# Kernel optimization log

Hardware: AMD Instinct MI355X
Metric: run time of the kernel (lower is better)

Reference implementation:

```python
import jax, jax.numpy as jnp
import numpy as np

N_NODES = 250_000
N_EDGES = 1_250_000
N_CRY = 50_000
EMB = 200
FEA = 64
HID = 256
N_GRAPH = 3
ELEM_HEADS = 3
CRY_HEADS = 3


def _simple_net(x, w1, b1, w2, b2):
    # SimpleNetwork([d_in, 256, d_out]): Linear -> LeakyReLU -> Linear
    h = jax.nn.leaky_relu(x @ w1 + b1, negative_slope=0.01)
    return h @ w2 + b2


def setup_inputs() -> dict:
    key = jax.random.key(0)
    ks = jax.random.split(key, 32)
    s = 0.05
    inp = {
        # weights strictly positive (fractional stoichiometry weights)
        "elem_weights": jax.random.uniform(ks[0], (N_NODES, 1), jnp.float32) * 0.9 + 0.05,
        "elem_fea": jax.random.normal(ks[1], (N_NODES, EMB), jnp.float32),
        "self_fea_idx": jax.random.randint(ks[2], (N_EDGES,), 0, N_NODES),
        "nbr_fea_idx": jax.random.randint(ks[3], (N_EDGES,), 0, N_NODES),
        "cry_elem_idx": jnp.sort(jax.random.randint(ks[4], (N_NODES,), 0, N_CRY)),
        # embedding: Linear(EMB, FEA-1)
        "emb_w": jax.random.normal(ks[5], (EMB, FEA - 1), jnp.float32) * s,
        "emb_b": jnp.zeros((FEA - 1,), jnp.float32),
        # graph-layer attention heads (n_graph, elem_heads, ...)
        "g_gate_w1": jax.random.normal(ks[6], (N_GRAPH, ELEM_HEADS, 2 * FEA, HID), jnp.float32) * s,
        "g_gate_b1": jnp.zeros((N_GRAPH, ELEM_HEADS, HID), jnp.float32),
        "g_gate_w2": jax.random.normal(ks[7], (N_GRAPH, ELEM_HEADS, HID, 1), jnp.float32) * s,
        "g_gate_b2": jnp.zeros((N_GRAPH, ELEM_HEADS, 1), jnp.float32),
        "g_msg_w1": jax.random.normal(ks[8], (N_GRAPH, ELEM_HEADS, 2 * FEA, HID), jnp.float32) * s,
        "g_msg_b1": jnp.zeros((N_GRAPH, ELEM_HEADS, HID), jnp.float32),
        "g_msg_w2": jax.random.normal(ks[9], (N_GRAPH, ELEM_HEADS, HID, FEA), jnp.float32) * s,
        "g_msg_b2": jnp.zeros((N_GRAPH, ELEM_HEADS, FEA), jnp.float32),
        "g_pow": jax.random.normal(ks[10], (N_GRAPH, ELEM_HEADS), jnp.float32),
        # crystal pooling heads
        "c_gate_w1": jax.random.normal(ks[11], (CRY_HEADS, FEA, HID), jnp.float32) * s,
        "c_gate_b1": jnp.zeros((CRY_HEADS, HID), jnp.float32),
        "c_gate_w2": jax.random.normal(ks[12], (CRY_HEADS, HID, 1), jnp.float32) * s,
        "c_gate_b2": jnp.zeros((CRY_HEADS, 1), jnp.float32),
        "c_msg_w1": jax.random.normal(ks[13], (CRY_HEADS, FEA, HID), jnp.float32) * s,
        "c_msg_b1": jnp.zeros((CRY_HEADS, HID), jnp.float32),
        "c_msg_w2": jax.random.normal(ks[14], (CRY_HEADS, HID, FEA), jnp.float32) * s,
        "c_msg_b2": jnp.zeros((CRY_HEADS, FEA), jnp.float32),
        "c_pow": jax.random.normal(ks[15], (CRY_HEADS,), jnp.float32),
    }
    return inp


def _attn_pool(fea, weights, index, num_segments, gw1, gb1, gw2, gb2, mw1, mb1, mw2, mb2, p):
    # WeightedAttentionPooling: scatter-softmax with (weights ** pow) factor
    gate = _simple_net(fea, gw1, gb1, gw2, gb2)                       # (E, 1)
    gmax = jax.ops.segment_max(gate, index, num_segments=num_segments)
    gate = (weights ** p) * jnp.exp(gate - gmax[index])
    den = jax.ops.segment_sum(gate, index, num_segments=num_segments)
    gate = gate / (den[index] + 1e-10)
    msg = _simple_net(fea, mw1, mb1, mw2, mb2)                        # (E, FEA)
    return jax.ops.segment_sum(gate * msg, index, num_segments=num_segments)


def reference(elem_weights, elem_fea, self_fea_idx, nbr_fea_idx, cry_elem_idx,
              emb_w, emb_b,
              g_gate_w1, g_gate_b1, g_gate_w2, g_gate_b2,
              g_msg_w1, g_msg_b1, g_msg_w2, g_msg_b2, g_pow,
              c_gate_w1, c_gate_b1, c_gate_w2, c_gate_b2,
              c_msg_w1, c_msg_b1, c_msg_w2, c_msg_b2, c_pow):
    n = elem_fea.shape[0]
    x = elem_fea @ emb_w + emb_b                                      # (N, FEA-1)
    x = jnp.concatenate([x, elem_weights], axis=1)                    # (N, FEA)
    w_nbr = elem_weights[nbr_fea_idx]                                 # (M, 1)
    for l in range(g_pow.shape[0]):
        fea = jnp.concatenate([x[self_fea_idx], x[nbr_fea_idx]], axis=1)  # (M, 2*FEA)
        heads = []
        for h in range(g_pow.shape[1]):
            heads.append(_attn_pool(
                fea, w_nbr, self_fea_idx, n,
                g_gate_w1[l, h], g_gate_b1[l, h], g_gate_w2[l, h], g_gate_b2[l, h],
                g_msg_w1[l, h], g_msg_b1[l, h], g_msg_w2[l, h], g_msg_b2[l, h],
                g_pow[l, h]))
        x = jnp.mean(jnp.stack(heads), axis=0) + x                    # residual
    heads = []
    for h in range(c_pow.shape[0]):
        heads.append(_attn_pool(
            x, elem_weights, cry_elem_idx, N_CRY,
            c_gate_w1[h], c_gate_b1[h], c_gate_w2[h], c_gate_b2[h],
            c_msg_w1[h], c_msg_b1[h], c_msg_w2[h], c_msg_b2[h],
            c_pow[h]))
    return jnp.mean(jnp.stack(heads), axis=0)                         # (C, FEA)
```

## Files before the change

### kernel.cpp

```cpp
#include <hip/hip_runtime.h>
#include <math.h>

#define NN 250000
#define NE 1250000
#define NC 50000
#define EMBD 200
#define NCH 245
#define NBLK 22000
#define SSTR ((size_t)NBLK * 64)

typedef unsigned int u32;
typedef unsigned short u16;
typedef short s16x8 __attribute__((ext_vector_type(8)));
typedef float f32x4 __attribute__((ext_vector_type(4)));

__device__ __forceinline__ u16 f2bf(float f) {
    u32 u = __float_as_uint(f);
    return (u16)((u + 0x7FFFu + ((u >> 16) & 1u)) >> 16);
}
__device__ __forceinline__ float bf2f(u16 u) { return __uint_as_float(((u32)u) << 16); }
__device__ __forceinline__ u32 cvtpk(float lo, float hi) {
    u32 r;
    asm("v_cvt_pk_bf16_f32 %0, %1, %2" : "=v"(r) : "v"(lo), "v"(hi));
    return r;
}
__device__ __forceinline__ float lrelu(float v) { return v > 0.f ? v : 0.01f * v; }
__device__ __forceinline__ u32 encf(float f) {
    u32 u = __float_as_uint(f);
    return (u & 0x80000000u) ? ~u : (u | 0x80000000u);
}
__device__ __forceinline__ float decf(u32 k) {
    return __uint_as_float((k & 0x80000000u) ? (k ^ 0x80000000u) : ~k);
}

__global__ void k_pack(const float* __restrict__ src, u16* __restrict__ dst,
                       int K, int N, int nheads)
{
    const int t = blockIdx.x * 256 + threadIdx.x;
    const int F = (K / 32) * (N / 16);
    if (t >= nheads * F * 64) return;
    const int lane = t & 63;
    const int fh = t >> 6;
    const int f = fh % F, head = fh / F;
    const int ng = f % (N / 16), ks = f / (N / 16);
    const int q = lane >> 4, c = lane & 15;
    const float* s = src + (size_t)head * K * N;
    u16 o[8];
    #pragma unroll
    for (int i = 0; i < 8; ++i)
        o[i] = f2bf(s[(size_t)(32 * ks + 8 * q + i) * N + 16 * ng + c]);
    uint4 v;
    v.x = (u32)o[0] | ((u32)o[1] << 16);
    v.y = (u32)o[2] | ((u32)o[3] << 16);
    v.z = (u32)o[4] | ((u32)o[5] << 16);
    v.w = (u32)o[6] | ((u32)o[7] << 16);
    *(uint4*)(dst + (size_t)head * K * N + ((size_t)f * 64 + lane) * 8) = v;
}

__global__ void k_packe(const float* __restrict__ src, u16* __restrict__ dst)
{
    const int t = blockIdx.x * 256 + threadIdx.x;
    if (t >= 28 * 64) return;
    const int lane = t & 63, f = t >> 6;
    const int ng = f & 3, ks = f >> 2;
    const int q = lane >> 4, c = lane & 15;
    u16 o[8];
    #pragma unroll
    for (int i = 0; i < 8; ++i) {
        const int kr = 32 * ks + 8 * q + i;
        const int col = 16 * ng + c;
        o[i] = (kr < EMBD && col < 63) ? f2bf(src[kr * 63 + col]) : (u16)0;
    }
    uint4 v;
    v.x = (u32)o[0] | ((u32)o[1] << 16);
    v.y = (u32)o[2] | ((u32)o[3] << 16);
    v.z = (u32)o[4] | ((u32)o[5] << 16);
    v.w = (u32)o[6] | ((u32)o[7] << 16);
    *(uint4*)(dst + ((size_t)f * 64 + lane) * 8) = v;
}

__global__ void k_pack2(const float* __restrict__ src, u16* __restrict__ dst, int nheads)
{
    const int t = blockIdx.x * 256 + threadIdx.x;
    const int F = 32;
    if (t >= nheads * F * 64) return;
    const int lane = t & 63;
    const int fh = t >> 6;
    const int f = fh % F, head = fh / F;
    const int ks2 = f >> 2, ng = f & 3;
    const int q = lane >> 4, c = lane & 15;
    const int half = ks2 >> 2, k2l = ks2 & 3;
    const float* s = src + (size_t)head * 256 * 64;
    u16 o[8];
    #pragma unroll
    for (int i = 0; i < 8; ++i) {
        const int pl = 32 * k2l + 8 * q + i;
        const int krow = (pl >> 5) * 64 + (2 * half + (pl & 1)) * 16 + ((pl >> 1) & 15);
        o[i] = f2bf(s[(size_t)krow * 64 + 16 * ng + c]);
    }
    uint4 v;
    v.x = (u32)o[0] | ((u32)o[1] << 16);
    v.y = (u32)o[2] | ((u32)o[3] << 16);
    v.z = (u32)o[4] | ((u32)o[5] << 16);
    v.w = (u32)o[6] | ((u32)o[7] << 16);
    *(uint4*)(dst + (size_t)head * 256 * 64 + ((size_t)f * 64 + lane) * 8) = v;
}

__global__ __launch_bounds__(256) void k_embed_mm(
    const float* __restrict__ elem_fea, const float* __restrict__ elem_w,
    const u16* __restrict__ webp, const float* __restrict__ emb_b,
    float* __restrict__ x, u16* __restrict__ xbf)
{
    __shared__ __align__(16) u16 Ahi[64 * 256];
    __shared__ __align__(16) u16 Alo[64 * 256];
    const int tid = threadIdx.x;
    const int n0 = blockIdx.x * 64;

    for (int i = tid; i < 64 * 3; i += 256) {
        const int row = i / 3, j = 25 + i % 3;
        uint4 z; z.x = 0; z.y = 0; z.z = 0; z.w = 0;
        *(uint4*)((char*)Ahi + row * 512 + ((j ^ (row & 7)) * 16)) = z;
        *(uint4*)((char*)Alo + row * 512 + ((j ^ (row & 7)) * 16)) = z;
    }
    for (int i = tid; i < 64 * 50; i += 256) {
        const int row = i / 50, f4 = i % 50;
        const int node = min(n0 + row, NN - 1);
        float4 v = *(const float4*)(elem_fea + (size_t)node * EMBD + f4 * 4);
        const u16 h0 = f2bf(v.x), h1 = f2bf(v.y), h2 = f2bf(v.z), h3 = f2bf(v.w);
        uint2 hi, lo;
        hi.x = (u32)h0 | ((u32)h1 << 16);
        hi.y = (u32)h2 | ((u32)h3 << 16);
        lo.x = (u32)f2bf(v.x - bf2f(h0)) | ((u32)f2bf(v.y - bf2f(h1)) << 16);
        lo.y = (u32)f2bf(v.z - bf2f(h2)) | ((u32)f2bf(v.w - bf2f(h3)) << 16);
        const int off = row * 512 + (((f4 >> 1) ^ (row & 7)) * 16) + (f4 & 1) * 8;
        *(uint2*)((char*)Ahi + off) = hi;
        *(uint2*)((char*)Alo + off) = lo;
    }
    __syncthreads();

    const int w = tid >> 6, lane = tid & 63, q = lane >> 4, c = lane & 15;
    s16x8 B[7];
    #pragma unroll
    for (int ks = 0; ks < 7; ++ks)
        B[ks] = *(const s16x8*)(webp + ((size_t)(ks * 4 + w) * 64 + lane) * 8);
    f32x4 acc[4];
    #pragma unroll
    for (int m = 0; m < 4; ++m) acc[m] = 0.f;
    #pragma unroll
    for (int ks = 0; ks < 7; ++ks) {
        #pragma unroll
        for (int m = 0; m < 4; ++m) {
            const int row = m * 16 + c;
            const int g = (ks * 4 + q) ^ (row & 7);
            s16x8 ah = *(const s16x8*)((const char*)Ahi + row * 512 + g * 16);
            s16x8 al = *(const s16x8*)((const char*)Alo + row * 512 + g * 16);
            acc[m] = __builtin_amdgcn_mfma_f32_16x16x32_bf16(ah, B[ks], acc[m], 0, 0, 0);
            acc[m] = __builtin_amdgcn_mfma_f32_16x16x32_bf16(al, B[ks], acc[m], 0, 0, 0);
        }
    }
    const int col = w * 16 + c;
    const float bv = (col < 63) ? emb_b[col] : 0.f;
    #pragma unroll
    for (int m = 0; m < 4; ++m)
        #pragma unroll
        for (int r = 0; r < 4; ++r) {
            const int node = n0 + m * 16 + q * 4 + r;
            if (node < NN) {
                const float val = (col < 63) ? acc[m][r] + bv : elem_w[node];
                x[(size_t)node * 64 + col] = val;
                xbf[(size_t)node * 64 + col] = f2bf(val);
            }
        }
}

__global__ void k_deg(const int* __restrict__ self_idx, int* __restrict__ deg) {
    int e = blockIdx.x * 256 + threadIdx.x;
    if (e < NE) atomicAdd(&deg[self_idx[e]], 1);
}

__global__ void k_nodepack(const int* __restrict__ deg, int* __restrict__ nstart,
                           int* __restrict__ ctotal)
{
    __shared__ int sdeg[1024];
    __shared__ int sst[1024];
    const int c0 = blockIdx.x << 10;
    const int cnt = min(1024, NN - c0);
    for (int i = threadIdx.x; i < cnt; i += 64) sdeg[i] = deg[c0 + i];
    __syncthreads();
    if (threadIdx.x == 0) {
        int cur = 0;
        for (int i = 0; i < cnt; ++i) {
            int d = sdeg[i];
            if (d > 0 && ((cur & 63) + d > 64)) cur = (cur + 63) & ~63;
            sst[i] = cur;
            cur += d;
        }
        ctotal[blockIdx.x] = (cur + 63) & ~63;
    }
    __syncthreads();
    for (int i = threadIdx.x; i < cnt; i += 64) nstart[c0 + i] = sst[i];
}

__global__ void k_chunkscan(const int* __restrict__ ctotal, int* __restrict__ cbase) {
    __shared__ int s[256];
    int t = threadIdx.x;
    int v = (t < NCH) ? ctotal[t] : 0;
    s[t] = v;
    __syncthreads();
    for (int off = 1; off < 256; off <<= 1) {
        int add = (t >= off) ? s[t - off] : 0;
        __syncthreads();
        s[t] += add;
        __syncthreads();
    }
    if (t < NCH) cbase[t] = s[t] - v;
}

__global__ void k_fill(const int* __restrict__ self_idx, const int* __restrict__ nstart,
                       const int* __restrict__ cbase, int* __restrict__ cursor,
                       int* __restrict__ eslot)
{
    int e = blockIdx.x * 256 + threadIdx.x;
    if (e >= NE) return;
    int n = self_idx[e];
    int r = atomicAdd(&cursor[n], 1);
    eslot[cbase[n >> 10] + nstart[n] + r] = e;
}

__global__ __launch_bounds__(256, 3) void k_lgate(
    const u16* __restrict__ xbf, const int* __restrict__ eslot,
    const int* __restrict__ sidx, const int* __restrict__ nidx,
    const float* __restrict__ elem_w,
    const u16* __restrict__ gw1p, const float* __restrict__ gb1,
    const float* __restrict__ gw2, const float* __restrict__ gpw,
    float* __restrict__ sgf_out)
{
    __shared__ __align__(16) u16 sA[64 * 128];
    __shared__ float sg[4][64];
    __shared__ float gfin[64], tval[64];
    __shared__ float swn[64];
    __shared__ int   snid[64];
    __shared__ short srs[64], sre[64];
    const int tid = threadIdx.x;
    const int base = blockIdx.x * 64;
    if (eslot[base] < 0) return;

    if (tid < 64) {
        int e = eslot[base + tid];
        snid[tid] = (e >= 0) ? sidx[e] : -1;
        swn[tid] = (e >= 0) ? elem_w[nidx[e]] : 1.f;
    }
    for (int i = tid; i < 64 * 16; i += 256) {
        const int row = i >> 4, g = i & 15;
        const int e = eslot[base + row];
        uint4 v; v.x = 0; v.y = 0; v.z = 0; v.w = 0;
        if (e >= 0) {
            const int node = (g < 8) ? sidx[e] : nidx[e];
            v = *(const uint4*)(xbf + (size_t)node * 64 + (g & 7) * 8);
        }
        *(uint4*)((char*)sA + row * 256 + ((g ^ (row & 7)) * 16)) = v;
    }
    __syncthreads();
    if (tid < 64) {
        int n = snid[tid];
        int rs = tid, re = tid + 1;
        if (n >= 0) {
            while (rs > 0 && snid[rs - 1] == n) --rs;
            while (re < 64 && snid[re] == n) ++re;
        }
        srs[tid] = (short)rs; sre[tid] = (short)re;
    }

    const int w = tid >> 6, lane = tid & 63, q = lane >> 4, c = lane & 15;

    #pragma unroll 1
    for (int h = 0; h < 3; ++h) {
        float part[4][4];
        #pragma unroll
        for (int m = 0; m < 4; ++m)
            #pragma unroll
            for (int r = 0; r < 4; ++r) part[m][r] = 0.f;
        const u16* wp = gw1p + (size_t)h * 128 * 256;
        #pragma unroll 1
        for (int half = 0; half < 2; ++half) {
            s16x8 B1[4][2];
            #pragma unroll
            for (int ks = 0; ks < 4; ++ks)
                #pragma unroll
                for (int n2 = 0; n2 < 2; ++n2)
                    B1[ks][n2] = *(const s16x8*)(wp + ((size_t)(ks * 16 + w * 4 + half * 2 + n2) * 64 + lane) * 8);
            f32x4 acc[4][2];
            #pragma unroll
            for (int m = 0; m < 4; ++m) { acc[m][0] = 0.f; acc[m][1] = 0.f; }
            __builtin_amdgcn_s_setprio(1);
            #pragma unroll
            for (int ks = 0; ks < 4; ++ks) {
                s16x8 a[4];
                #pragma unroll
                for (int m = 0; m < 4; ++m) {
                    const int row = m * 16 + c;
                    a[m] = *(const s16x8*)((const char*)sA + row * 256 + (((ks * 4 + q) ^ (row & 7)) * 16));
                }
                #pragma unroll
                for (int n2 = 0; n2 < 2; ++n2)
                    #pragma unroll
                    for (int m = 0; m < 4; ++m)
                        acc[m][n2] = __builtin_amdgcn_mfma_f32_16x16x32_bf16(a[m], B1[ks][n2], acc[m][n2], 0, 0, 0);
            }
            __builtin_amdgcn_s_setprio(0);
            #pragma unroll
            for (int n2 = 0; n2 < 2; ++n2) {
                const int col = w * 64 + (half * 2 + n2) * 16 + c;
                const float b1v = gb1[h * 256 + col];
                const float w2v = gw2[h * 256 + col];
                #pragma unroll
                for (int m = 0; m < 4; ++m)
                    #pragma unroll
                    for (int r = 0; r < 4; ++r)
                        part[m][r] += lrelu(acc[m][n2][r] + b1v) * w2v;
            }
        }
        #pragma unroll
        for (int off = 1; off < 16; off <<= 1)
            #pragma unroll
            for (int m = 0; m < 4; ++m)
                #pragma unroll
                for (int r = 0; r < 4; ++r)
                    part[m][r] += __shfl_xor(part[m][r], off, 64);
        if (c == 0) {
            #pragma unroll
            for (int m = 0; m < 4; ++m)
                #pragma unroll
                for (int r = 0; r < 4; ++r)
                    sg[w][m * 16 + q * 4 + r] = part[m][r];
        }
        __syncthreads();
        if (tid < 64)
            gfin[tid] = (snid[tid] >= 0) ? sg[0][tid] + sg[1][tid] + sg[2][tid] + sg[3][tid] : -1e30f;
        __syncthreads();
        if (tid < 64) {
            const int rs = srs[tid], re = sre[tid];
            float m = -1e30f;
            for (int j = rs; j < re; ++j) m = fmaxf(m, gfin[j]);
            tval[tid] = (snid[tid] >= 0) ? powf(swn[tid], gpw[h]) * expf(gfin[tid] - m) : 0.f;
        }
        __syncthreads();
        if (tid < 64) {
            const int rs = srs[tid], re = sre[tid];
            float d = 1e-10f;
            for (int j = rs; j < re; ++j) d += tval[j];
            sgf_out[SSTR * h + base + tid] = tval[tid] / d;
        }
        __syncthreads();
    }
}

__global__ __launch_bounds__(256, 3) void k_lmsg(
    const u16* __restrict__ xbf, const int* __restrict__ eslot,
    const int* __restrict__ sidx, const int* __restrict__ nidx,
    const u16* __restrict__ mw1p, const float* __restrict__ mb1,
    const u16* __restrict__ mw2p, const float* __restrict__ mb2,
    const float* __restrict__ sgf_in, float* __restrict__ pooled)
{
    __shared__ __align__(16) u16 sA[64 * 128];
    __shared__ __align__(16) u16 sH[64 * 128];
    __shared__ float sgfl[64][3];
    __shared__ int   snid[64];
    __shared__ short srs[64], sre[64];
    const int tid = threadIdx.x;
    const int base = blockIdx.x * 64;
    if (eslot[base] < 0) return;

    if (tid < 64) {
        int e = eslot[base + tid];
        snid[tid] = (e >= 0) ? sidx[e] : -1;
    }
    if (tid < 192) {
        const int row = tid / 3, h = tid % 3;
        sgfl[row][h] = sgf_in[SSTR * h + base + row];
    }
    for (int i = tid; i < 64 * 16; i += 256) {
        const int row = i >> 4, g = i & 15;
        const int e = eslot[base + row];
        uint4 v; v.x = 0; v.y = 0; v.z = 0; v.w = 0;
        if (e >= 0) {
            const int node = (g < 8) ? sidx[e] : nidx[e];
            v = *(const uint4*)(xbf + (size_t)node * 64 + (g & 7) * 8);
        }
        *(uint4*)((char*)sA + row * 256 + ((g ^ (row & 7)) * 16)) = v;
    }
    __syncthreads();
    if (tid < 64) {
        int n = snid[tid];
        int rs = tid, re = tid + 1;
        if (n >= 0) {
            while (rs > 0 && snid[rs - 1] == n) --rs;
            while (re < 64 && snid[re] == n) ++re;
        }
        srs[tid] = (short)rs; sre[tid] = (short)re;
    }

    const int w = tid >> 6, lane = tid & 63, q = lane >> 4, c = lane & 15;
    float wacc[4][4];
    #pragma unroll
    for (int m = 0; m < 4; ++m)
        #pragma unroll
        for (int r = 0; r < 4; ++r) wacc[m][r] = 0.f;

    #pragma unroll 1
    for (int h = 0; h < 3; ++h) {
        const u16* wp = mw1p + (size_t)h * 128 * 256;
        #pragma unroll 1
        for (int half = 0; half < 2; ++half) {
            s16x8 B1[4][2];
            #pragma unroll
            for (int ks = 0; ks < 4; ++ks)
                #pragma unroll
                for (int n2 = 0; n2 < 2; ++n2)
                    B1[ks][n2] = *(const s16x8*)(wp + ((size_t)(ks * 16 + w * 4 + half * 2 + n2) * 64 + lane) * 8);
            f32x4 acc[4][2];
            #pragma unroll
            for (int m = 0; m < 4; ++m) { acc[m][0] = 0.f; acc[m][1] = 0.f; }
            __builtin_amdgcn_s_setprio(1);
            #pragma unroll
            for (int ks = 0; ks < 4; ++ks) {
                s16x8 a[4];
                #pragma unroll
                for (int m = 0; m < 4; ++m) {
                    const int row = m * 16 + c;
                    a[m] = *(const s16x8*)((const char*)sA + row * 256 + (((ks * 4 + q) ^ (row & 7)) * 16));
                }
                #pragma unroll
                for (int n2 = 0; n2 < 2; ++n2)
                    #pragma unroll
                    for (int m = 0; m < 4; ++m)
                        acc[m][n2] = __builtin_amdgcn_mfma_f32_16x16x32_bf16(a[m], B1[ks][n2], acc[m][n2], 0, 0, 0);
            }
            __builtin_amdgcn_s_setprio(0);

            __syncthreads();
            const float b1a = mb1[h * 256 + w * 64 + (half * 2 + 0) * 16 + c];
            const float b1b = mb1[h * 256 + w * 64 + (half * 2 + 1) * 16 + c];
            #pragma unroll
            for (int m = 0; m < 4; ++m)
                #pragma unroll
                for (int r = 0; r < 4; ++r) {
                    const int row = m * 16 + q * 4 + r;
                    const u32 pk = cvtpk(lrelu(acc[m][0][r] + b1a), lrelu(acc[m][1][r] + b1b));
                    *(u32*)((char*)sH + row * 256 + (((w * 4 + (c >> 2)) ^ (row & 7)) * 16) + (c & 3) * 4) = pk;
                }
            s16x8 B2[4];
            #pragma unroll
            for (int k2 = 0; k2 < 4; ++k2)
                B2[k2] = *(const s16x8*)(mw2p + (size_t)h * 256 * 64 + ((size_t)((half * 4 + k2) * 4 + w) * 64 + lane) * 8);
            __syncthreads();

            f32x4 acc2[4];
            #pragma unroll
            for (int m = 0; m < 4; ++m) acc2[m] = 0.f;
            __builtin_amdgcn_s_setprio(1);
            #pragma unroll
            for (int k2 = 0; k2 < 4; ++k2) {
                #pragma unroll
                for (int m2 = 0; m2 < 4; ++m2) {
                    const int row = m2 * 16 + c;
                    s16x8 a2 = *(const s16x8*)((const char*)sH + row * 256 + (((k2 * 4 + q) ^ (row & 7)) * 16));
                    acc2[m2] = __builtin_amdgcn_mfma_f32_16x16x32_bf16(a2, B2[k2], acc2[m2], 0, 0, 0);
                }
            }
            __builtin_amdgcn_s_setprio(0);
            const float b2v = half ? mb2[h * 64 + w * 16 + c] : 0.f;
            #pragma unroll
            for (int m2 = 0; m2 < 4; ++m2)
                #pragma unroll
                for (int r = 0; r < 4; ++r) {
                    const int row = m2 * 16 + q * 4 + r;
                    wacc[m2][r] += (acc2[m2][r] + b2v) * sgfl[row][h];
                }
        }
        __syncthreads();
    }

    float* waccL = (float*)sH;
    #pragma unroll
    for (int m = 0; m < 4; ++m)
        #pragma unroll
        for (int r = 0; r < 4; ++r)
            waccL[(m * 16 + q * 4 + r) * 64 + w * 16 + c] = wacc[m][r];
    __syncthreads();
    {
        const int col = tid & 63, grp = tid >> 6;
        for (int i = grp; i < 64; i += 4) {
            const int n = snid[i];
            if (n >= 0 && srs[i] == (short)i) {
                float s = 0.f;
                const int re = sre[i];
                for (int j = i; j < re; ++j) s += waccL[j * 64 + col];
                pooled[(size_t)n * 64 + col] = s * (1.f / 3.f);
            }
        }
    }
}

__global__ void k_mirror2(float* __restrict__ x, const float* __restrict__ pooled,
                          u16* __restrict__ xbf, int n4)
{
    int i = blockIdx.x * 256 + threadIdx.x;
    if (i >= n4) return;
    float4 xv = *(const float4*)(x + (size_t)i * 4);
    float4 pv = *(const float4*)(pooled + (size_t)i * 4);
    xv.x += pv.x; xv.y += pv.y; xv.z += pv.z; xv.w += pv.w;
    *(float4*)(x + (size_t)i * 4) = xv;
    uint2 o;
    o.x = cvtpk(xv.x, xv.y);
    o.y = cvtpk(xv.z, xv.w);
    *(uint2*)(xbf + (size_t)i * 4) = o;
}

template<int KD, bool GATHER>
__global__ __launch_bounds__(256, 3) void k_gate(
    const u16* __restrict__ xbf, const int* __restrict__ sidx, const int* __restrict__ nidx,
    const int* __restrict__ scat, const u16* __restrict__ w1p,
    const float* __restrict__ b1g, const float* __restrict__ w2g,
    float* __restrict__ gate_out, u32* __restrict__ gmax, int nrows, size_t gstride)
{
    constexpr int KS = KD / 32;
    constexpr int RB = KD * 2;
    constexpr int G  = KD / 8;
    __shared__ __align__(16) u16 sA[64 * KD];
    __shared__ float sg[4][64];
    const int tid = threadIdx.x;
    const int r0 = blockIdx.x * 64;
    const int rem = min(64, nrows - r0);

    for (int i = tid; i < 64 * G; i += 256) {
        const int row = i / G, g = i % G;
        const int rr = (row < rem) ? row : 0;
        uint4 v;
        if (GATHER) {
            const int node = (g < G / 2) ? sidx[r0 + rr] : nidx[r0 + rr];
            v = *(const uint4*)(xbf + (size_t)node * 64 + (g & (G / 2 - 1)) * 8);
        } else {
            v = *(const uint4*)(xbf + (size_t)(r0 + rr) * 64 + g * 8);
        }
        *(uint4*)((char*)sA + row * RB + ((g ^ (row & 7)) * 16)) = v;
    }
    __syncthreads();

    const int w = tid >> 6, lane = tid & 63, q = lane >> 4, c = lane & 15;

    #pragma unroll 1
    for (int h = 0; h < 3; ++h) {
        float part[4][4];
        #pragma unroll
        for (int m = 0; m < 4; ++m)
            #pragma unroll
            for (int r = 0; r < 4; ++r) part[m][r] = 0.f;
        const u16* wp = w1p + (size_t)h * KD * 256;
        #pragma unroll 1
        for (int half = 0; half < 2; ++half) {
            s16x8 B1[KS][2];
            #pragma unroll
            for (int ks = 0; ks < KS; ++ks)
                #pragma unroll
                for (int n2 = 0; n2 < 2; ++n2)
                    B1[ks][n2] = *(const s16x8*)(wp + ((size_t)(ks * 16 + w * 4 + half * 2 + n2) * 64 + lane) * 8);
            f32x4 acc[4][2];
            #pragma unroll
            for (int m = 0; m < 4; ++m) { acc[m][0] = 0.f; acc[m][1] = 0.f; }
            __builtin_amdgcn_s_setprio(1);
            #pragma unroll
            for (int ks = 0; ks < KS; ++ks) {
                s16x8 a[4];
                #pragma unroll
                for (int m = 0; m < 4; ++m) {
                    const int row = m * 16 + c;
                    a[m] = *(const s16x8*)((const char*)sA + row * RB + (((ks * 4 + q) ^ (row & 7)) * 16));
                }
                #pragma unroll
                for (int n2 = 0; n2 < 2; ++n2)
                    #pragma unroll
                    for (int m = 0; m < 4; ++m)
                        acc[m][n2] = __builtin_amdgcn_mfma_f32_16x16x32_bf16(a[m], B1[ks][n2], acc[m][n2], 0, 0, 0);
            }
            __builtin_amdgcn_s_setprio(0);
            #pragma unroll
            for (int n2 = 0; n2 < 2; ++n2) {
                const int col = w * 64 + (half * 2 + n2) * 16 + c;
                const float b1v = b1g[h * 256 + col];
                const float w2v = w2g[h * 256 + col];
                #pragma unroll
                for (int m = 0; m < 4; ++m)
                    #pragma unroll
                    for (int r = 0; r < 4; ++r)
                        part[m][r] += lrelu(acc[m][n2][r] + b1v) * w2v;
            }
        }
        #pragma unroll
        for (int off = 1; off < 16; off <<= 1)
            #pragma unroll
            for (int m = 0; m < 4; ++m)
                #pragma unroll
                for (int r = 0; r < 4; ++r)
                    part[m][r] += __shfl_xor(part[m][r], off, 64);
        if (c == 0) {
            #pragma unroll
            for (int m = 0; m < 4; ++m)
                #pragma unroll
                for (int r = 0; r < 4; ++r)
                    sg[w][m * 16 + q * 4 + r] = part[m][r];
        }
        __syncthreads();
        if (tid < rem) {
            const float gv = sg[0][tid] + sg[1][tid] + sg[2][tid] + sg[3][tid];
            gate_out[gstride * h + r0 + tid] = gv;
            atomicMax(&gmax[scat[r0 + tid] * 3 + h], encf(gv));
        }
        __syncthreads();
    }
}

template<int KD, bool GATHER>
__global__ __launch_bounds__(256, 3) void k_msg(
    const u16* __restrict__ xbf, const int* __restrict__ sidx, const int* __restrict__ nidx,
    const int* __restrict__ scat, const u16* __restrict__ w1p, const float* __restrict__ b1g,
    const u16* __restrict__ w2p, const float* __restrict__ b2g,
    const float* __restrict__ tbuf, const float* __restrict__ den,
    float* __restrict__ outp, int nrows, size_t gstride)
{
    constexpr int KS = KD / 32;
    constexpr int RB = KD * 2;
    constexpr int G  = KD / 8;
    __shared__ __align__(16) u16 sA[64 * KD];
    __shared__ __align__(16) u16 sH[64 * 128];
    __shared__ float sgf[64][3];
    __shared__ int ssi[64];
    const int tid = threadIdx.x;
    const int r0 = blockIdx.x * 64;
    const int rem = min(64, nrows - r0);

    for (int i = tid; i < 64 * G; i += 256) {
        const int row = i / G, g = i % G;
        const int rr = (row < rem) ? row : 0;
        uint4 v;
        if (GATHER) {
            const int node = (g < G / 2) ? sidx[r0 + rr] : nidx[r0 + rr];
            v = *(const uint4*)(xbf + (size_t)node * 64 + (g & (G / 2 - 1)) * 8);
        } else {
            v = *(const uint4*)(xbf + (size_t)(r0 + rr) * 64 + g * 8);
        }
        *(uint4*)((char*)sA + row * RB + ((g ^ (row & 7)) * 16)) = v;
    }
    if (tid < 64) ssi[tid] = (tid < rem) ? scat[r0 + tid] : 0;
    if (tid < 192) {
        const int row = tid / 3, h = tid % 3;
        if (row < rem) {
            const int s = scat[r0 + row] * 3 + h;
            sgf[row][h] = tbuf[gstride * h + r0 + row] / (den[s] + 1e-10f);
        } else {
            sgf[row][h] = 0.f;
        }
    }
    __syncthreads();

    const int w = tid >> 6, lane = tid & 63, q = lane >> 4, c = lane & 15;
    float wacc[4][4];
    #pragma unroll
    for (int m = 0; m < 4; ++m)
        #pragma unroll
        for (int r = 0; r < 4; ++r) wacc[m][r] = 0.f;

    #pragma unroll 1
    for (int h = 0; h < 3; ++h) {
        const u16* wp = w1p + (size_t)h * KD * 256;
        #pragma unroll 1
        for (int half = 0; half < 2; ++half) {
            s16x8 B1[KS][2];
            #pragma unroll
            for (int ks = 0; ks < KS; ++ks)
                #pragma unroll
                for (int n2 = 0; n2 < 2; ++n2)
                    B1[ks][n2] = *(const s16x8*)(wp + ((size_t)(ks * 16 + w * 4 + half * 2 + n2) * 64 + lane) * 8);
            f32x4 acc[4][2];
            #pragma unroll
            for (int m = 0; m < 4; ++m) { acc[m][0] = 0.f; acc[m][1] = 0.f; }
            __builtin_amdgcn_s_setprio(1);
            #pragma unroll
            for (int ks = 0; ks < KS; ++ks) {
                s16x8 a[4];
                #pragma unroll
                for (int m = 0; m < 4; ++m) {
                    const int row = m * 16 + c;
                    a[m] = *(const s16x8*)((const char*)sA + row * RB + (((ks * 4 + q) ^ (row & 7)) * 16));
                }
                #pragma unroll
                for (int n2 = 0; n2 < 2; ++n2)
                    #pragma unroll
                    for (int m = 0; m < 4; ++m)
                        acc[m][n2] = __builtin_amdgcn_mfma_f32_16x16x32_bf16(a[m], B1[ks][n2], acc[m][n2], 0, 0, 0);
            }
            __builtin_amdgcn_s_setprio(0);

            __syncthreads();
            const float b1a = b1g[h * 256 + w * 64 + (half * 2 + 0) * 16 + c];
            const float b1b = b1g[h * 256 + w * 64 + (half * 2 + 1) * 16 + c];
            #pragma unroll
            for (int m = 0; m < 4; ++m)
                #pragma unroll
                for (int r = 0; r < 4; ++r) {
                    const int row = m * 16 + q * 4 + r;
                    const u32 pk = cvtpk(lrelu(acc[m][0][r] + b1a), lrelu(acc[m][1][r] + b1b));
                    *(u32*)((char*)sH + row * 256 + (((w * 4 + (c >> 2)) ^ (row & 7)) * 16) + (c & 3) * 4) = pk;
                }
            s16x8 B2[4];
            #pragma unroll
            for (int k2 = 0; k2 < 4; ++k2)
                B2[k2] = *(const s16x8*)(w2p + (size_t)h * 256 * 64 + ((size_t)((half * 4 + k2) * 4 + w) * 64 + lane) * 8);
            __syncthreads();

            f32x4 acc2[4];
            #pragma unroll
            for (int m = 0; m < 4; ++m) acc2[m] = 0.f;
            __builtin_amdgcn_s_setprio(1);
            #pragma unroll
            for (int k2 = 0; k2 < 4; ++k2) {
                #pragma unroll
                for (int m2 = 0; m2 < 4; ++m2) {
                    const int row = m2 * 16 + c;
                    s16x8 a2 = *(const s16x8*)((const char*)sH + row * 256 + (((k2 * 4 + q) ^ (row & 7)) * 16));
                    acc2[m2] = __builtin_amdgcn_mfma_f32_16x16x32_bf16(a2, B2[k2], acc2[m2], 0, 0, 0);
                }
            }
            __builtin_amdgcn_s_setprio(0);
            const float b2v = half ? b2g[h * 64 + w * 16 + c] : 0.f;
            #pragma unroll
            for (int m2 = 0; m2 < 4; ++m2)
                #pragma unroll
                for (int r = 0; r < 4; ++r) {
                    const int row = m2 * 16 + q * 4 + r;
                    wacc[m2][r] += (acc2[m2][r] + b2v) * sgf[row][h];
                }
        }
    }
    #pragma unroll
    for (int m = 0; m < 4; ++m)
        #pragma unroll
        for (int r = 0; r < 4; ++r) {
            const int row = m * 16 + q * 4 + r;
            if (row < rem)
                atomicAdd(&outp[(size_t)ssi[row] * 64 + w * 16 + c], wacc[m][r] * (1.f / 3.f));
        }
}

__global__ void k_seg_exp(float* __restrict__ gate_t, const int* __restrict__ idx,
                          const int* __restrict__ wi, const float* __restrict__ elem_w,
                          const float* __restrict__ pw, const u32* __restrict__ gmax,
                          float* __restrict__ den, int n, size_t gstride)
{
    int e = blockIdx.x * blockDim.x + threadIdx.x;
    if (e >= n) return;
    int s = idx[e] * 3;
    float wgt = elem_w[wi ? wi[e] : e];
    #pragma unroll
    for (int h = 0; h < 3; ++h) {
        float gm = decf(gmax[s + h]);
        float t = powf(wgt, pw[h]) * expf(gate_t[gstride * h + e] - gm);
        gate_t[gstride * h + e] = t;
        atomicAdd(&den[s + h], t);
    }
}

extern "C" void kernel_launch(void* const* d_in, const int* in_sizes, int n_in,
                              void* d_out, int out_size, void* d_ws, size_t ws_size,
                              hipStream_t stream)
{
    const float* elem_w   = (const float*)d_in[0];
    const float* elem_fea = (const float*)d_in[1];
    const int*   self_idx = (const int*)d_in[2];
    const int*   nbr_idx  = (const int*)d_in[3];
    const int*   cry_idx  = (const int*)d_in[4];
    const float* emb_w    = (const float*)d_in[5];
    const float* emb_b    = (const float*)d_in[6];
    const float* gg_w1    = (const float*)d_in[7];
    const float* gg_b1    = (const float*)d_in[8];
    const float* gg_w2    = (const float*)d_in[9];
    const float* gm_w1    = (const float*)d_in[11];
    const float* gm_b1    = (const float*)d_in[12];
    const float* gm_w2    = (const float*)d_in[13];
    const float* gm_b2    = (const float*)d_in[14];
    const float* g_pow    = (const float*)d_in[15];
    const float* cg_w1    = (const float*)d_in[16];
    const float* cg_b1    = (const float*)d_in[17];
    const float* cg_w2    = (const float*)d_in[18];
    const float* cm_w1    = (const float*)d_in[20];
    const float* cm_b1    = (const float*)d_in[21];
    const float* cm_w2    = (const float*)d_in[22];
    const float* cm_b2    = (const float*)d_in[23];
    const float* c_pow    = (const float*)d_in[24];

    char* wsp = (char*)d_ws;
    size_t off = 0;
    auto alloc = [&](size_t b) { char* p = wsp + off; off += (b + 255) & ~(size_t)255; return p; };
    float* x      = (float*)alloc((size_t)NN * 64 * 4);
    float* pooled = (float*)alloc((size_t)NN * 64 * 4);
    u16*   xbf    = (u16*)  alloc((size_t)NN * 64 * 2);
    float* sgf    = (float*)alloc((size_t)3 * SSTR * 4);
    float* gate_t = (float*)alloc((size_t)NN * 3 * 4);
    float* cden   = (float*)alloc((size_t)NC * 3 * 4);
    u32*   cgmax  = (u32*)  alloc((size_t)NC * 3 * 4);
    int* deg    = (int*)alloc((size_t)NN * 4);
    int* nstart = (int*)alloc((size_t)NN * 4);
    int* cursor = (int*)alloc((size_t)NN * 4);
    int* ctotal = (int*)alloc((size_t)NCH * 4);
    int* cbase  = (int*)alloc((size_t)NCH * 4);
    int* eslot  = (int*)alloc((size_t)NBLK * 64 * 4);
    u16* wg1p = (u16*)alloc((size_t)9 * 128 * 256 * 2);
    u16* wm1p = (u16*)alloc((size_t)9 * 128 * 256 * 2);
    u16* wm2p = (u16*)alloc((size_t)9 * 256 * 64 * 2);
    u16* cg1p = (u16*)alloc((size_t)3 * 64 * 256 * 2);
    u16* cm1p = (u16*)alloc((size_t)3 * 64 * 256 * 2);
    u16* cm2p = (u16*)alloc((size_t)3 * 256 * 64 * 2);
    u16* webp = (u16*)alloc((size_t)224 * 64 * 2);

    auto pack = [&](const float* s, u16* d, int K, int N, int H) {
        int tot = H * (K / 32) * (N / 16) * 64;
        k_pack<<<(tot + 255) / 256, 256, 0, stream>>>(s, d, K, N, H);
    };
    pack(gg_w1, wg1p, 128, 256, 9);
    pack(gm_w1, wm1p, 128, 256, 9);
    pack(cg_w1, cg1p, 64, 256, 3);
    pack(cm_w1, cm1p, 64, 256, 3);
    k_pack2<<<(9 * 32 * 64 + 255) / 256, 256, 0, stream>>>(gm_w2, wm2p, 9);
    k_pack2<<<(3 * 32 * 64 + 255) / 256, 256, 0, stream>>>(cm_w2, cm2p, 3);
    k_packe<<<7, 256, 0, stream>>>(emb_w, webp);

    hipMemsetAsync(deg, 0, (size_t)NN * 4, stream);
    hipMemsetAsync(cursor, 0, (size_t)NN * 4, stream);
    hipMemsetAsync(eslot, 0xFF, (size_t)NBLK * 64 * 4, stream);
    k_deg<<<(NE + 255) / 256, 256, 0, stream>>>(self_idx, deg);
    k_nodepack<<<NCH, 64, 0, stream>>>(deg, nstart, ctotal);
    k_chunkscan<<<1, 256, 0, stream>>>(ctotal, cbase);
    k_fill<<<(NE + 255) / 256, 256, 0, stream>>>(self_idx, nstart, cbase, cursor, eslot);

    k_embed_mm<<<(NN + 63) / 64, 256, 0, stream>>>(elem_fea, elem_w, webp, emb_b, x, xbf);

    for (int l = 0; l < 3; ++l) {
        hipMemsetAsync(pooled, 0, (size_t)NN * 64 * 4, stream);
        k_lgate<<<NBLK, 256, 0, stream>>>(
            xbf, eslot, self_idx, nbr_idx, elem_w,
            wg1p + (size_t)l * 3 * 128 * 256, gg_b1 + l * 768, gg_w2 + l * 768, g_pow + l * 3,
            sgf);
        k_lmsg<<<NBLK, 256, 0, stream>>>(
            xbf, eslot, self_idx, nbr_idx,
            wm1p + (size_t)l * 3 * 128 * 256, gm_b1 + l * 768,
            wm2p + (size_t)l * 3 * 256 * 64, gm_b2 + l * 192, sgf, pooled);
        k_mirror2<<<(NN * 64 / 4 + 255) / 256, 256, 0, stream>>>(x, pooled, xbf, NN * 64 / 4);
    }

    hipMemsetAsync(cgmax, 0, (size_t)NC * 3 * 4, stream);
    hipMemsetAsync(cden, 0, (size_t)NC * 3 * 4, stream);
    hipMemsetAsync(d_out, 0, (size_t)NC * 64 * 4, stream);
    const int GN = (NN + 63) / 64;
    k_gate<64, false><<<GN, 256, 0, stream>>>(
        xbf, nullptr, nullptr, cry_idx, cg1p, cg_b1, cg_w2, gate_t, cgmax, NN, (size_t)NN);
    k_seg_exp<<<(NN + 255) / 256, 256, 0, stream>>>(
        gate_t, cry_idx, nullptr, elem_w, c_pow, cgmax, cden, NN, (size_t)NN);
    k_msg<64, false><<<GN, 256, 0, stream>>>(
        xbf, nullptr, nullptr, cry_idx, cm1p, cm_b1, cm2p, cm_b2,
        gate_t, cden, (float*)d_out, NN, (size_t)NN);
}
```

Before: 4.231 ms.

## Fuse graph-layer gate and message kernels into one per-edge-block kernel

Merges the gate-computation kernel and the message kernel of each graph layer into a single kernel. The edge-block gather of source and neighbour features into shared memory happens once instead of twice, and the normalized gate weights stay in shared memory instead of going through a global scratch buffer. The cost is a larger shared-memory footprint and more register pressure in one kernel, which may reduce occupancy.

Result: slower. 4.802 ms (+13.5%).

```diff
diff --git a/kernel.cpp b/kernel.cpp
--- a/kernel.cpp
+++ b/kernel.cpp
@@ -7,7 +7,6 @@
 #define EMBD 200
 #define NCH 245
 #define NBLK 22000
-#define SSTR ((size_t)NBLK * 64)
 
 typedef unsigned int u32;
 typedef unsigned short u16;
@@ -227,17 +226,20 @@
     eslot[cbase[n >> 10] + nstart[n] + r] = e;
 }
 
-__global__ __launch_bounds__(256, 3) void k_lgate(
+__global__ __launch_bounds__(256, 3) void k_layer(
     const u16* __restrict__ xbf, const int* __restrict__ eslot,
     const int* __restrict__ sidx, const int* __restrict__ nidx,
     const float* __restrict__ elem_w,
     const u16* __restrict__ gw1p, const float* __restrict__ gb1,
     const float* __restrict__ gw2, const float* __restrict__ gpw,
-    float* __restrict__ sgf_out)
+    const u16* __restrict__ mw1p, const float* __restrict__ mb1,
+    const u16* __restrict__ mw2p, const float* __restrict__ mb2,
+    float* __restrict__ pooled)
 {
     __shared__ __align__(16) u16 sA[64 * 128];
+    __shared__ __align__(16) u16 sH[64 * 128];
     __shared__ float sg[4][64];
-    __shared__ float gfin[64], tval[64];
+    __shared__ float gfin[64], tval[64], sgfl[64];
     __shared__ float swn[64];
     __shared__ int   snid[64];
     __shared__ short srs[64], sre[64];
@@ -272,67 +274,74 @@
     }
 
     const int w = tid >> 6, lane = tid & 63, q = lane >> 4, c = lane & 15;
+    float wacc[4][4];
+    #pragma unroll
+    for (int m = 0; m < 4; ++m)
+        #pragma unroll
+        for (int r = 0; r < 4; ++r) wacc[m][r] = 0.f;
 
     #pragma unroll 1
     for (int h = 0; h < 3; ++h) {
-        float part[4][4];
-        #pragma unroll
-        for (int m = 0; m < 4; ++m)
-            #pragma unroll
-            for (int r = 0; r < 4; ++r) part[m][r] = 0.f;
-        const u16* wp = gw1p + (size_t)h * 128 * 256;
-        #pragma unroll 1
-        for (int half = 0; half < 2; ++half) {
-            s16x8 B1[4][2];
-            #pragma unroll
-            for (int ks = 0; ks < 4; ++ks)
-                #pragma unroll
-                for (int n2 = 0; n2 < 2; ++n2)
-                    B1[ks][n2] = *(const s16x8*)(wp + ((size_t)(ks * 16 + w * 4 + half * 2 + n2) * 64 + lane) * 8);
-            f32x4 acc[4][2];
-            #pragma unroll
-            for (int m = 0; m < 4; ++m) { acc[m][0] = 0.f; acc[m][1] = 0.f; }
-            __builtin_amdgcn_s_setprio(1);
-            #pragma unroll
-            for (int ks = 0; ks < 4; ++ks) {
-                s16x8 a[4];
-                #pragma unroll
-                for (int m = 0; m < 4; ++m) {
-                    const int row = m * 16 + c;
-                    a[m] = *(const s16x8*)((const char*)sA + row * 256 + (((ks * 4 + q) ^ (row & 7)) * 16));
+        {
+            float part[4][4];
+            #pragma unroll
+            for (int m = 0; m < 4; ++m)
+                #pragma unroll
+                for (int r = 0; r < 4; ++r) part[m][r] = 0.f;
+            const u16* wp = gw1p + (size_t)h * 128 * 256;
+            #pragma unroll 1
+            for (int half = 0; half < 2; ++half) {
+                s16x8 B1[4][2];
+                #pragma unroll
+                for (int ks = 0; ks < 4; ++ks)
+                    #pragma unroll
+                    for (int n2 = 0; n2 < 2; ++n2)
+                        B1[ks][n2] = *(const s16x8*)(wp + ((size_t)(ks * 16 + w * 4 + half * 2 + n2) * 64 + lane) * 8);
+                f32x4 acc[4][2];
+                #pragma unroll
+                for (int m = 0; m < 4; ++m) { acc[m][0] = 0.f; acc[m][1] = 0.f; }
+                __builtin_amdgcn_s_setprio(1);
+                #pragma unroll
+                for (int ks = 0; ks < 4; ++ks) {
+                    s16x8 a[4];
+                    #pragma unroll
+                    for (int m = 0; m < 4; ++m) {
+                        const int row = m * 16 + c;
+                        a[m] = *(const s16x8*)((const char*)sA + row * 256 + (((ks * 4 + q) ^ (row & 7)) * 16));
+                    }
+                    #pragma unroll
+                    for (int n2 = 0; n2 < 2; ++n2)
+                        #pragma unroll
+                        for (int m = 0; m < 4; ++m)
+                            acc[m][n2] = __builtin_amdgcn_mfma_f32_16x16x32_bf16(a[m], B1[ks][n2], acc[m][n2], 0, 0, 0);
                 }
-                #pragma unroll
-                for (int n2 = 0; n2 < 2; ++n2)
+                __builtin_amdgcn_s_setprio(0);
+                #pragma unroll
+                for (int n2 = 0; n2 < 2; ++n2) {
+                    const int col = w * 64 + (half * 2 + n2) * 16 + c;
+                    const float b1v = gb1[h * 256 + col];
+                    const float w2v = gw2[h * 256 + col];
                     #pragma unroll
                     for (int m = 0; m < 4; ++m)
-                        acc[m][n2] = __builtin_amdgcn_mfma_f32_16x16x32_bf16(a[m], B1[ks][n2], acc[m][n2], 0, 0, 0);
+                        #pragma unroll
+                        for (int r = 0; r < 4; ++r)
+                            part[m][r] += lrelu(acc[m][n2][r] + b1v) * w2v;
+                }
             }
-            __builtin_amdgcn_s_setprio(0);
-            #pragma unroll
-            for (int n2 = 0; n2 < 2; ++n2) {
-                const int col = w * 64 + (half * 2 + n2) * 16 + c;
-                const float b1v = gb1[h * 256 + col];
-                const float w2v = gw2[h * 256 + col];
+            #pragma unroll
+            for (int off = 1; off < 16; off <<= 1)
                 #pragma unroll
                 for (int m = 0; m < 4; ++m)
                     #pragma unroll
                     for (int r = 0; r < 4; ++r)
-                        part[m][r] += lrelu(acc[m][n2][r] + b1v) * w2v;
+                        part[m][r] += __shfl_xor(part[m][r], off, 64);
+            if (c == 0) {
+                #pragma unroll
+                for (int m = 0; m < 4; ++m)
+                    #pragma unroll
+                    for (int r = 0; r < 4; ++r)
+                        sg[w][m * 16 + q * 4 + r] = part[m][r];
             }
-        }
-        #pragma unroll
-        for (int off = 1; off < 16; off <<= 1)
-            #pragma unroll
-            for (int m = 0; m < 4; ++m)
-                #pragma unroll
-                for (int r = 0; r < 4; ++r)
-                    part[m][r] += __shfl_xor(part[m][r], off, 64);
-        if (c == 0) {
-            #pragma unroll
-            for (int m = 0; m < 4; ++m)
-                #pragma unroll
-                for (int r = 0; r < 4; ++r)
-                    sg[w][m * 16 + q * 4 + r] = part[m][r];
         }
         __syncthreads();
         if (tid < 64)
@@ -349,134 +358,80 @@
             const int rs = srs[tid], re = sre[tid];
             float d = 1e-10f;
             for (int j = rs; j < re; ++j) d += tval[j];
-            sgf_out[SSTR * h + base + tid] = tval[tid] / d;
+            sgfl[tid] = tval[tid] / d;
         }
         __syncthreads();
-    }
-}
-
-__global__ __launch_bounds__(256, 3) void k_lmsg(
-    const u16* __restrict__ xbf, const int* __restrict__ eslot,
-    const int* __restrict__ sidx, const int* __restrict__ nidx,
-    const u16* __restrict__ mw1p, const float* __restrict__ mb1,
-    const u16* __restrict__ mw2p, const float* __restrict__ mb2,
-    const float* __restrict__ sgf_in, float* __restrict__ pooled)
-{
-    __shared__ __align__(16) u16 sA[64 * 128];
-    __shared__ __align__(16) u16 sH[64 * 128];
-    __shared__ float sgfl[64][3];
-    __shared__ int   snid[64];
-    __shared__ short srs[64], sre[64];
-    const int tid = threadIdx.x;
-    const int base = blockIdx.x * 64;
-    if (eslot[base] < 0) return;
-
-    if (tid < 64) {
-        int e = eslot[base + tid];
-        snid[tid] = (e >= 0) ? sidx[e] : -1;
-    }
-    if (tid < 192) {
-        const int row = tid / 3, h = tid % 3;
-        sgfl[row][h] = sgf_in[SSTR * h + base + row];
-    }
-    for (int i = tid; i < 64 * 16; i += 256) {
-        const int row = i >> 4, g = i & 15;
-        const int e = eslot[base + row];
-        uint4 v; v.x = 0; v.y = 0; v.z = 0; v.w = 0;
-        if (e >= 0) {
-            const int node = (g < 8) ? sidx[e] : nidx[e];
-            v = *(const uint4*)(xbf + (size_t)node * 64 + (g & 7) * 8);
-        }
-        *(uint4*)((char*)sA + row * 256 + ((g ^ (row & 7)) * 16)) = v;
-    }
-    __syncthreads();
-    if (tid < 64) {
-        int n = snid[tid];
-        int rs = tid, re = tid + 1;
-        if (n >= 0) {
-            while (rs > 0 && snid[rs - 1] == n) --rs;
-            while (re < 64 && snid[re] == n) ++re;
-        }
-        srs[tid] = (short)rs; sre[tid] = (short)re;
-    }
-
-    const int w = tid >> 6, lane = tid & 63, q = lane >> 4, c = lane & 15;
-    float wacc[4][4];
-    #pragma unroll
-    for (int m = 0; m < 4; ++m)
-        #pragma unroll
-        for (int r = 0; r < 4; ++r) wacc[m][r] = 0.f;
-
-    #pragma unroll 1
-    for (int h = 0; h < 3; ++h) {
-        const u16* wp = mw1p + (size_t)h * 128 * 256;
-        #pragma unroll 1
-        for (int half = 0; half < 2; ++half) {
-            s16x8 B1[4][2];
-            #pragma unroll
-            for (int ks = 0; ks < 4; ++ks)
-                #pragma unroll
-                for (int n2 = 0; n2 < 2; ++n2)
-                    B1[ks][n2] = *(const s16x8*)(wp + ((size_t)(ks * 16 + w * 4 + half * 2 + n2) * 64 + lane) * 8);
-            f32x4 acc[4][2];
-            #pragma unroll
-            for (int m = 0; m < 4; ++m) { acc[m][0] = 0.f; acc[m][1] = 0.f; }
-            __builtin_amdgcn_s_setprio(1);
-            #pragma unroll
-            for (int ks = 0; ks < 4; ++ks) {
-                s16x8 a[4];
-                #pragma unroll
-                for (int m = 0; m < 4; ++m) {
-                    const int row = m * 16 + c;
-                    a[m] = *(const s16x8*)((const char*)sA + row * 256 + (((ks * 4 + q) ^ (row & 7)) * 16));
+
+        {
+            const u16* wp = mw1p + (size_t)h * 128 * 256;
+            #pragma unroll 1
+            for (int half = 0; half < 2; ++half) {
+                s16x8 B1[4][2];
+                #pragma unroll
+                for (int ks = 0; ks < 4; ++ks)
+                    #pragma unroll
+                    for (int n2 = 0; n2 < 2; ++n2)
+                        B1[ks][n2] = *(const s16x8*)(wp + ((size_t)(ks * 16 + w * 4 + half * 2 + n2) * 64 + lane) * 8);
+                f32x4 acc[4][2];
+                #pragma unroll
+                for (int m = 0; m < 4; ++m) { acc[m][0] = 0.f; acc[m][1] = 0.f; }
+                __builtin_amdgcn_s_setprio(1);
+                #pragma unroll
+                for (int ks = 0; ks < 4; ++ks) {
+                    s16x8 a[4];
+                    #pragma unroll
+                    for (int m = 0; m < 4; ++m) {
+                        const int row = m * 16 + c;
+                        a[m] = *(const s16x8*)((const char*)sA + row * 256 + (((ks * 4 + q) ^ (row & 7)) * 16));
+                    }
+                    #pragma unroll
+                    for (int n2 = 0; n2 < 2; ++n2)
+                        #pragma unroll
+                        for (int m = 0; m < 4; ++m)
+                            acc[m][n2] = __builtin_amdgcn_mfma_f32_16x16x32_bf16(a[m], B1[ks][n2], acc[m][n2], 0, 0, 0);
                 }
-                #pragma unroll
-                for (int n2 = 0; n2 < 2; ++n2)
-                    #pragma unroll
-                    for (int m = 0; m < 4; ++m)
-                        acc[m][n2] = __builtin_amdgcn_mfma_f32_16x16x32_bf16(a[m], B1[ks][n2], acc[m][n2], 0, 0, 0);
+                __builtin_amdgcn_s_setprio(0);
+
+                __syncthreads();
+                const float b1a = mb1[h * 256 + w * 64 + (half * 2 + 0) * 16 + c];
+                const float b1b = mb1[h * 256 + w * 64 + (half * 2 + 1) * 16 + c];
+                #pragma unroll
+                for (int m = 0; m < 4; ++m)
+                    #pragma unroll
+                    for (int r = 0; r < 4; ++r) {
+                        const int row = m * 16 + q * 4 + r;
+                        const u32 pk = cvtpk(lrelu(acc[m][0][r] + b1a), lrelu(acc[m][1][r] + b1b));
+                        *(u32*)((char*)sH + row * 256 + (((w * 4 + (c >> 2)) ^ (row & 7)) * 16) + (c & 3) * 4) = pk;
+                    }
+                s16x8 B2[4];
+                #pragma unroll
+                for (int k2 = 0; k2 < 4; ++k2)
+                    B2[k2] = *(const s16x8*)(mw2p + (size_t)h * 256 * 64 + ((size_t)((half * 4 + k2) * 4 + w) * 64 + lane) * 8);
+                __syncthreads();
+
+                f32x4 acc2[4];
+                #pragma unroll
+                for (int m = 0; m < 4; ++m) acc2[m] = 0.f;
+                __builtin_amdgcn_s_setprio(1);
+                #pragma unroll
+                for (int k2 = 0; k2 < 4; ++k2) {
+                    #pragma unroll
+                    for (int m2 = 0; m2 < 4; ++m2) {
+                        const int row = m2 * 16 + c;
+                        s16x8 a2 = *(const s16x8*)((const char*)sH + row * 256 + (((k2 * 4 + q) ^ (row & 7)) * 16));
+                        acc2[m2] = __builtin_amdgcn_mfma_f32_16x16x32_bf16(a2, B2[k2], acc2[m2], 0, 0, 0);
+                    }
+                }
+                __builtin_amdgcn_s_setprio(0);
+                const float b2v = half ? mb2[h * 64 + w * 16 + c] : 0.f;
+                #pragma unroll
+                for (int m2 = 0; m2 < 4; ++m2)
+                    #pragma unroll
+                    for (int r = 0; r < 4; ++r) {
+                        const int row = m2 * 16 + q * 4 + r;
+                        wacc[m2][r] += (acc2[m2][r] + b2v) * sgfl[row];
+                    }
             }
-            __builtin_amdgcn_s_setprio(0);
-
-            __syncthreads();
-            const float b1a = mb1[h * 256 + w * 64 + (half * 2 + 0) * 16 + c];
-            const float b1b = mb1[h * 256 + w * 64 + (half * 2 + 1) * 16 + c];
-            #pragma unroll
-            for (int m = 0; m < 4; ++m)
-                #pragma unroll
-                for (int r = 0; r < 4; ++r) {
-                    const int row = m * 16 + q * 4 + r;
-                    const u32 pk = cvtpk(lrelu(acc[m][0][r] + b1a), lrelu(acc[m][1][r] + b1b));
-                    *(u32*)((char*)sH + row * 256 + (((w * 4 + (c >> 2)) ^ (row & 7)) * 16) + (c & 3) * 4) = pk;
-                }
-            s16x8 B2[4];
-            #pragma unroll
-            for (int k2 = 0; k2 < 4; ++k2)
-                B2[k2] = *(const s16x8*)(mw2p + (size_t)h * 256 * 64 + ((size_t)((half * 4 + k2) * 4 + w) * 64 + lane) * 8);
-            __syncthreads();
-
-            f32x4 acc2[4];
-            #pragma unroll
-            for (int m = 0; m < 4; ++m) acc2[m] = 0.f;
-            __builtin_amdgcn_s_setprio(1);
-            #pragma unroll
-            for (int k2 = 0; k2 < 4; ++k2) {
-                #pragma unroll
-                for (int m2 = 0; m2 < 4; ++m2) {
-                    const int row = m2 * 16 + c;
-                    s16x8 a2 = *(const s16x8*)((const char*)sH + row * 256 + (((k2 * 4 + q) ^ (row & 7)) * 16));
-                    acc2[m2] = __builtin_amdgcn_mfma_f32_16x16x32_bf16(a2, B2[k2], acc2[m2], 0, 0, 0);
-                }
-            }
-            __builtin_amdgcn_s_setprio(0);
-            const float b2v = half ? mb2[h * 64 + w * 16 + c] : 0.f;
-            #pragma unroll
-            for (int m2 = 0; m2 < 4; ++m2)
-                #pragma unroll
-                for (int r = 0; r < 4; ++r) {
-                    const int row = m2 * 16 + q * 4 + r;
-                    wacc[m2][r] += (acc2[m2][r] + b2v) * sgfl[row][h];
-                }
         }
         __syncthreads();
     }
@@ -804,7 +759,6 @@
     float* x      = (float*)alloc((size_t)NN * 64 * 4);
     float* pooled = (float*)alloc((size_t)NN * 64 * 4);
     u16*   xbf    = (u16*)  alloc((size_t)NN * 64 * 2);
-    float* sgf    = (float*)alloc((size_t)3 * SSTR * 4);
     float* gate_t = (float*)alloc((size_t)NN * 3 * 4);
     float* cden   = (float*)alloc((size_t)NC * 3 * 4);
     u32*   cgmax  = (u32*)  alloc((size_t)NC * 3 * 4);
@@ -846,14 +800,11 @@
 
     for (int l = 0; l < 3; ++l) {
         hipMemsetAsync(pooled, 0, (size_t)NN * 64 * 4, stream);
-        k_lgate<<<NBLK, 256, 0, stream>>>(
+        k_layer<<<NBLK, 256, 0, stream>>>(
             xbf, eslot, self_idx, nbr_idx, elem_w,
             wg1p + (size_t)l * 3 * 128 * 256, gg_b1 + l * 768, gg_w2 + l * 768, g_pow + l * 3,
-            sgf);
-        k_lmsg<<<NBLK, 256, 0, stream>>>(
-            xbf, eslot, self_idx, nbr_idx,
             wm1p + (size_t)l * 3 * 128 * 256, gm_b1 + l * 768,
-            wm2p + (size_t)l * 3 * 256 * 64, gm_b2 + l * 192, sgf, pooled);
+            wm2p + (size_t)l * 3 * 256 * 64, gm_b2 + l * 192, pooled);
         k_mirror2<<<(NN * 64 / 4 + 255) / 256, 256, 0, stream>>>(x, pooled, xbf, NN * 64 / 4);
     }
 
```
